# Optimization experiments

Measured on AMD Instinct MI355X. Metric: run time of the kernel, lower is better.

## Reference

```python
import jax, jax.numpy as jnp
import numpy as np

N, E, IN, H, C, L = 40000, 640000, 256, 128, 64, 4
ALPHA, LAMB = 0.5, 1.0


def setup_inputs() -> dict:
    key = jax.random.key(0)
    ks = jax.random.split(key, 8)
    x = jax.random.normal(ks[0], (N, IN), jnp.float32)
    src = jax.random.randint(ks[1], (E,), 0, N, jnp.int32)
    dst = jax.random.randint(ks[2], (E,), 0, N, jnp.int32)
    s_in = 1.0 / np.sqrt(IN)
    s_h = 1.0 / np.sqrt(H)
    fc1_w = jax.random.normal(ks[3], (IN, H), jnp.float32) * s_in
    fc1_b = jnp.zeros((H,), jnp.float32)
    W1 = jax.random.normal(ks[4], (L, H, H), jnp.float32) * s_h   # GCN2Conv weight1 per layer
    W2 = jax.random.normal(ks[5], (L, H, H), jnp.float32) * s_h   # GCN2Conv weight2 (initial-residual proj)
    bgc = jnp.zeros((L, H), jnp.float32)                          # GCN2Conv bias per layer
    fc2_w = jax.random.normal(ks[6], (H, C), jnp.float32) * s_h
    fc2_b = jnp.zeros((C,), jnp.float32)
    return dict(x=x, fc1_w=fc1_w, fc1_b=fc1_b, W1=W1, W2=W2, bgc=bgc,
                fc2_w=fc2_w, fc2_b=fc2_b, src=src, dst=dst)


def reference(x, fc1_w, fc1_b, W1, W2, bgc, fc2_w, fc2_b, src, dst):
    ones = jnp.ones((E,), x.dtype)
    # symmetric 'both' normalization: deg_out^{-1/2} on src side, deg_in^{-1/2} on dst side
    deg_out = jnp.clip(jax.ops.segment_sum(ones, src, num_segments=N), 1.0)
    deg_in = jnp.clip(jax.ops.segment_sum(ones, dst, num_segments=N), 1.0)
    norm_s = (deg_out ** -0.5)[:, None]
    norm_d = (deg_in ** -0.5)[:, None]

    # feature_preprocess: dropout (eval = identity) -> fc1 -> relu
    h0 = jax.nn.relu(x @ fc1_w + fc1_b)          # [N, H]
    h = h0
    for l in range(L):
        beta = float(np.log(LAMB / (l + 1) + 1.0))
        identity = h
        # sparse neighbor aggregation (SpMM via gather + segment_sum)
        agg = jax.ops.segment_sum((h * norm_s)[src], dst, num_segments=N) * norm_d
        feat = (1.0 - ALPHA) * agg               # smoothed features
        f0 = ALPHA * h0                          # initial residual
        rst = (1.0 - beta) * (feat + f0) + beta * (feat @ W1[l] + f0 @ W2[l]) + bgc[l]
        h = jax.nn.relu(rst + identity)          # outer residual + activation (dropout eval = identity)
    return h @ fc2_w + fc2_b                     # [N, C]
```

## Files before the change

kernel.cpp:

```cpp
#include <hip/hip_runtime.h>
#include <math.h>

#define N_NODES 40000
#define N_EDGES 640000
#define IN_F 256
#define H_F 128
#define C_F 64
#define L_LAYERS 4
#define SCAN_BLKS 157
#define N_CHUNKS 32
#define CHUNK_E 20000
#define HIST_WORDS 10000

typedef short short8 __attribute__((ext_vector_type(8)));
typedef unsigned short ushort8 __attribute__((ext_vector_type(8)));
typedef float f32x4 __attribute__((ext_vector_type(4)));

__device__ inline short to_bf16(float f) {
    unsigned u = __builtin_bit_cast(unsigned, f);
    unsigned r = (u + 0x7FFFu + ((u >> 16) & 1u)) >> 16;
    return (short)r;
}
__device__ inline float bf16_to_f(unsigned short u) {
    unsigned v = ((unsigned)u) << 16;
    return __builtin_bit_cast(float, v);
}

__device__ inline int block_excl_scan(int v, int* wsum, int* tot) {
    int tid = threadIdx.x;
    int lane = tid & 63, wid = tid >> 6;
    int incl = v;
    #pragma unroll
    for (int off = 1; off < 64; off <<= 1) {
        int t = __shfl_up(incl, off, 64);
        if (lane >= off) incl += t;
    }
    if (lane == 63) wsum[wid] = incl;
    __syncthreads();
    int prefix = 0, total = 0;
    #pragma unroll
    for (int w = 0; w < 4; w++) {
        int s = wsum[w];
        if (w < wid) prefix += s;
        total += s;
    }
    *tot = total;
    return prefix + incl - v;
}

__global__ void prep_w(const float* __restrict__ fc1_w,
                       const float* __restrict__ W1, const float* __restrict__ W2,
                       const float* __restrict__ fc2_w,
                       short* __restrict__ fc1_wT, short* __restrict__ WcatT,
                       short* __restrict__ fc2_wT) {
    int i = blockIdx.x * 256 + threadIdx.x;
    if (i < 128 * 256) {
        int n = i >> 8, k = i & 255;
        fc1_wT[i] = to_bf16(fc1_w[k * H_F + n]);
    }
    if (i < 4 * 128 * 256) {
        int l = i >> 15; int r = i & 32767; int n = r >> 8; int k = r & 255;
        float w = (k < 128) ? W1[l * 16384 + k * H_F + n]
                            : W2[l * 16384 + (k - 128) * H_F + n];
        WcatT[i] = to_bf16(0.5f * w);
    }
    if (i < 64 * 128) {
        int n = i >> 7, k = i & 127;
        fc2_wT[i] = to_bf16(fc2_w[k * C_F + n]);
    }
}

#define CVT8(dstv, p) {                                                         \
    float4 _v0 = *(const float4*)(p); float4 _v1 = *(const float4*)((p) + 4);   \
    dstv[0] = to_bf16(_v0.x); dstv[1] = to_bf16(_v0.y);                         \
    dstv[2] = to_bf16(_v0.z); dstv[3] = to_bf16(_v0.w);                         \
    dstv[4] = to_bf16(_v1.x); dstv[5] = to_bf16(_v1.y);                         \
    dstv[6] = to_bf16(_v1.z); dstv[7] = to_bf16(_v1.w); }

__global__ __launch_bounds__(256) void hist_fc1(const int* __restrict__ src,
                                                const int* __restrict__ dst,
                                                int* __restrict__ chunk_dst,
                                                int* __restrict__ chunk_src,
                                                unsigned char* __restrict__ lrank8,
                                                const float* __restrict__ x,
                                                const short* __restrict__ wT,
                                                const float* __restrict__ b,
                                                unsigned short* __restrict__ h0b) {
    __shared__ int cntp[HIST_WORDS];
    int blk = blockIdx.x;
    if (blk < 64) {
        int role_dst = (blk < 32);
        int w = role_dst ? blk : blk - 32;
        const int* idx = role_dst ? dst : src;
        int base = w * CHUNK_E;
        for (int i = threadIdx.x; i < HIST_WORDS; i += 256) cntp[i] = 0;
        __syncthreads();
        if (role_dst) {
            for (int i = threadIdx.x; i < CHUNK_E; i += 256) {
                int d = idx[base + i];
                int sh = (d & 3) * 8;
                int old = atomicAdd(&cntp[d >> 2], 1 << sh);
                lrank8[base + i] = (unsigned char)((old >> sh) & 0xff);
            }
        } else {
            for (int i = threadIdx.x; i < CHUNK_E; i += 256) {
                int s = idx[base + i];
                atomicAdd(&cntp[s >> 2], 1 << ((s & 3) * 8));
            }
        }
        __syncthreads();
        int* outp = role_dst ? (chunk_dst + w * HIST_WORDS) : (chunk_src + w * HIST_WORDS);
        for (int i = threadIdx.x; i < HIST_WORDS; i += 256) outp[i] = cntp[i];
        return;
    }
    int bb = blk - 64;
    int tid = threadIdx.x;
    int wave = tid >> 6, lane = tid & 63;
    int m = lane & 15, quad = lane >> 4;
    int row = bb * 64 + wave * 16 + m;
    const float* xr = x + (size_t)row * IN_F + quad * 8;
    short8 afrag[8];
    #pragma unroll
    for (int ks = 0; ks < 8; ks++) {
        CVT8(afrag[ks], xr + ks * 32);
    }
    #pragma unroll
    for (int c = 0; c < 8; c += 2) {
        f32x4 acc0 = {0.f, 0.f, 0.f, 0.f};
        f32x4 acc1 = {0.f, 0.f, 0.f, 0.f};
        const short* b0p = wT + (size_t)(c * 16 + m) * IN_F + quad * 8;
        const short* b1p = b0p + 16 * IN_F;
        #pragma unroll
        for (int ks = 0; ks < 8; ks++) {
            short8 b0 = *(const short8*)(b0p + ks * 32);
            short8 b1 = *(const short8*)(b1p + ks * 32);
            acc0 = __builtin_amdgcn_mfma_f32_16x16x32_bf16(afrag[ks], b0, acc0, 0, 0, 0);
            acc1 = __builtin_amdgcn_mfma_f32_16x16x32_bf16(afrag[ks], b1, acc1, 0, 0, 0);
        }
        int col0 = c * 16 + m;
        int rbase = bb * 64 + wave * 16 + quad * 4;
        float bg0 = b[col0], bg1 = b[col0 + 16];
        #pragma unroll
        for (int r = 0; r < 4; r++) {
            size_t idx2 = (size_t)(rbase + r) * H_F + col0;
            float v0 = acc0[r] + bg0;
            float v1 = acc1[r] + bg1;
            v0 = v0 > 0.f ? v0 : 0.f;
            v1 = v1 > 0.f ? v1 : 0.f;
            h0b[idx2] = (unsigned short)to_bf16(v0);
            h0b[idx2 + 16] = (unsigned short)to_bf16(v1);
        }
    }
}

__global__ __launch_bounds__(256) void scan1(const int* __restrict__ chunk_dst,
                                             const int* __restrict__ chunk_src,
                                             unsigned short* __restrict__ base16,
                                             float* __restrict__ rsq_in,
                                             float* __restrict__ rsq_out,
                                             int* __restrict__ row_local,
                                             int* __restrict__ blk_sum) {
    __shared__ int wsum[4];
    int n = blockIdx.x * 256 + threadIdx.x;
    int deg_in = 0;
    if (n < N_NODES) {
        int word = n >> 2, sh = (n & 3) * 8;
        int run = 0;
        #pragma unroll 4
        for (int w = 0; w < N_CHUNKS; w++) {
            int v = (chunk_dst[w * HIST_WORDS + word] >> sh) & 0xff;
            base16[w * N_NODES + n] = (unsigned short)run;
            run += v;
        }
        deg_in = run;
        int so = 0;
        #pragma unroll 4
        for (int w = 0; w < N_CHUNKS; w++)
            so += (chunk_src[w * HIST_WORDS + word] >> sh) & 0xff;
        rsq_in[n] = 1.0f / sqrtf((float)(deg_in < 1 ? 1 : deg_in));
        rsq_out[n] = 1.0f / sqrtf((float)(so < 1 ? 1 : so));
    }
    int tot;
    int excl = block_excl_scan(deg_in, wsum, &tot);
    if (n < N_NODES) row_local[n] = excl;
    if (threadIdx.x == 0) blk_sum[blockIdx.x] = tot;
}

__global__ __launch_bounds__(256) void scan2(const int* __restrict__ blk_sum,
                                             int* __restrict__ blk_off) {
    __shared__ int wsum[4];
    int t = threadIdx.x;
    int v = (t < SCAN_BLKS) ? blk_sum[t] : 0;
    int tot;
    int excl = block_excl_scan(v, wsum, &tot);
    if (t < SCAN_BLKS) blk_off[t] = excl;
}

__global__ __launch_bounds__(256) void fill_fused(const int* __restrict__ src,
                                                  const int* __restrict__ dst,
                                                  const unsigned char* __restrict__ lrank8,
                                                  const unsigned short* __restrict__ base16,
                                                  const int* __restrict__ row_local,
                                                  const int* __restrict__ blk_off,
                                                  const float* __restrict__ rsq_in,
                                                  const float* __restrict__ rsq_out,
                                                  int* __restrict__ col,
                                                  float* __restrict__ wv,
                                                  int* __restrict__ row_ptr) {
    int blk = blockIdx.x;
    if (blk < 2500) {
        int e = blk * 256 + threadIdx.x;
        int w = e / CHUNK_E;
        int s = src[e], d = dst[e];
        int rp = blk_off[d >> 8] + row_local[d] + (int)base16[w * N_NODES + d]
               + (int)lrank8[e];
        col[rp] = s;
        wv[rp] = rsq_out[s] * rsq_in[d];
        return;
    }
    int n = (blk - 2500) * 256 + threadIdx.x;
    if (n < N_NODES) row_ptr[n] = blk_off[n >> 8] + row_local[n];
    if (blk == 2500 && threadIdx.x == 0) row_ptr[N_NODES] = N_EDGES;
}

__global__ __launch_bounds__(256) void spmm_kernel(const unsigned short* __restrict__ hb,
                                                   const int* __restrict__ row_ptr,
                                                   const int* __restrict__ col,
                                                   const float* __restrict__ wv,
                                                   unsigned short* __restrict__ aggb) {
    int wave = threadIdx.x >> 6, lane = threadIdx.x & 63;
    int slot = lane >> 4, fi = lane & 15;
    int n = blockIdx.x * 4 + wave;
    int e0 = row_ptr[n], e1 = row_ptr[n + 1];
    float a[8] = {};
    int e = e0 + slot;
    for (; e + 12 < e1; e += 16) {
        int c0 = col[e];      float w0 = wv[e];
        int c1 = col[e + 4];  float w1 = wv[e + 4];
        int c2 = col[e + 8];  float w2 = wv[e + 8];
        int c3 = col[e + 12]; float w3 = wv[e + 12];
        ushort8 u0 = *(const ushort8*)(hb + (size_t)c0 * H_F + fi * 8);
        ushort8 u1 = *(const ushort8*)(hb + (size_t)c1 * H_F + fi * 8);
        ushort8 u2 = *(const ushort8*)(hb + (size_t)c2 * H_F + fi * 8);
        ushort8 u3 = *(const ushort8*)(hb + (size_t)c3 * H_F + fi * 8);
        #pragma unroll
        for (int j = 0; j < 8; j++) {
            a[j] += w0 * bf16_to_f(u0[j]) + w1 * bf16_to_f(u1[j])
                  + w2 * bf16_to_f(u2[j]) + w3 * bf16_to_f(u3[j]);
        }
    }
    for (; e < e1; e += 4) {
        int c = col[e];
        float w = wv[e];
        ushort8 u = *(const ushort8*)(hb + (size_t)c * H_F + fi * 8);
        #pragma unroll
        for (int j = 0; j < 8; j++) a[j] += w * bf16_to_f(u[j]);
    }
    #pragma unroll
    for (int mask = 16; mask <= 32; mask <<= 1) {
        #pragma unroll
        for (int j = 0; j < 8; j++) a[j] += __shfl_xor(a[j], mask, 64);
    }
    if (slot == 0) {
        ushort8 r;
        #pragma unroll
        for (int j = 0; j < 8; j++) r[j] = (unsigned short)to_bf16(a[j]);
        *(ushort8*)(aggb + (size_t)n * H_F + fi * 8) = r;
    }
}

__global__ __launch_bounds__(256) void combine_mfma(const unsigned short* __restrict__ aggb,
                                                    const unsigned short* __restrict__ h0b,
                                                    const unsigned short* __restrict__ hb,
                                                    const short* __restrict__ wT,
                                                    const float* __restrict__ bgc,
                                                    float beta,
                                                    unsigned short* __restrict__ h_outb) {
    int tid = threadIdx.x;
    int wave = tid >> 6, lane = tid & 63;
    int m = lane & 15, quad = lane >> 4;
    int row = blockIdx.x * 64 + wave * 16 + m;
    const unsigned short* aggr = aggb + (size_t)row * H_F + quad * 8;
    const unsigned short* h0r  = h0b + (size_t)row * H_F + quad * 8;
    short8 afrag[8];
    #pragma unroll
    for (int ks = 0; ks < 4; ks++) {
        afrag[ks] = __builtin_bit_cast(short8, *(const ushort8*)(aggr + ks * 32));
        afrag[ks + 4] = __builtin_bit_cast(short8, *(const ushort8*)(h0r + ks * 32));
    }
    float omb = 1.f - beta;
    #pragma unroll
    for (int c = 0; c < 8; c += 2) {
        f32x4 acc0 = {0.f, 0.f, 0.f, 0.f};
        f32x4 acc1 = {0.f, 0.f, 0.f, 0.f};
        const short* b0p = wT + (size_t)(c * 16 + m) * 256 + quad * 8;
        const short* b1p = b0p + 16 * 256;
        #pragma unroll
        for (int ks = 0; ks < 8; ks++) {
            short8 b0 = *(const short8*)(b0p + ks * 32);
            short8 b1 = *(const short8*)(b1p + ks * 32);
            acc0 = __builtin_amdgcn_mfma_f32_16x16x32_bf16(afrag[ks], b0, acc0, 0, 0, 0);
            acc1 = __builtin_amdgcn_mfma_f32_16x16x32_bf16(afrag[ks], b1, acc1, 0, 0, 0);
        }
        int col0 = c * 16 + m;
        int rbase = blockIdx.x * 64 + wave * 16 + quad * 4;
        float bg0 = bgc[col0], bg1 = bgc[col0 + 16];
        #pragma unroll
        for (int r = 0; r < 4; r++) {
            size_t idx = (size_t)(rbase + r) * H_F + col0;
            float s0 = 0.5f * (bf16_to_f(aggb[idx]) + bf16_to_f(h0b[idx]));
            float s1 = 0.5f * (bf16_to_f(aggb[idx + 16]) + bf16_to_f(h0b[idx + 16]));
            float v0 = omb * s0 + beta * acc0[r] + bg0 + bf16_to_f(hb[idx]);
            float v1 = omb * s1 + beta * acc1[r] + bg1 + bf16_to_f(hb[idx + 16]);
            v0 = v0 > 0.f ? v0 : 0.f;
            v1 = v1 > 0.f ? v1 : 0.f;
            h_outb[idx] = (unsigned short)to_bf16(v0);
            h_outb[idx + 16] = (unsigned short)to_bf16(v1);
        }
    }
}

__global__ __launch_bounds__(256) void fc2_mfma(const unsigned short* __restrict__ hb,
                                                const short* __restrict__ wT,
                                                const float* __restrict__ b,
                                                float* __restrict__ out) {
    int tid = threadIdx.x;
    int wave = tid >> 6, lane = tid & 63;
    int m = lane & 15, quad = lane >> 4;
    int row = blockIdx.x * 64 + wave * 16 + m;
    const unsigned short* hr = hb + (size_t)row * H_F + quad * 8;
    short8 afrag[4];
    #pragma unroll
    for (int ks = 0; ks < 4; ks++) {
        afrag[ks] = __builtin_bit_cast(short8, *(const ushort8*)(hr + ks * 32));
    }
    #pragma unroll
    for (int c = 0; c < 4; c += 2) {
        f32x4 acc0 = {0.f, 0.f, 0.f, 0.f};
        f32x4 acc1 = {0.f, 0.f, 0.f, 0.f};
        const short* b0p = wT + (size_t)(c * 16 + m) * H_F + quad * 8;
        const short* b1p = b0p + 16 * H_F;
        #pragma unroll
        for (int ks = 0; ks < 4; ks++) {
            short8 b0 = *(const short8*)(b0p + ks * 32);
            short8 b1 = *(const short8*)(b1p + ks * 32);
            acc0 = __builtin_amdgcn_mfma_f32_16x16x32_bf16(afrag[ks], b0, acc0, 0, 0, 0);
            acc1 = __builtin_amdgcn_mfma_f32_16x16x32_bf16(afrag[ks], b1, acc1, 0, 0, 0);
        }
        int col0 = c * 16 + m;
        int rbase = blockIdx.x * 64 + wave * 16 + quad * 4;
        float bg0 = b[col0], bg1 = b[col0 + 16];
        #pragma unroll
        for (int r = 0; r < 4; r++) {
            size_t idx = (size_t)(rbase + r) * C_F + col0;
            out[idx] = acc0[r] + bg0;
            out[idx + 16] = acc1[r] + bg1;
        }
    }
}

extern "C" void kernel_launch(void* const* d_in, const int* in_sizes, int n_in,
                              void* d_out, int out_size, void* d_ws, size_t ws_size,
                              hipStream_t stream) {
    const float* x     = (const float*)d_in[0];
    const float* fc1_w = (const float*)d_in[1];
    const float* fc1_b = (const float*)d_in[2];
    const float* W1    = (const float*)d_in[3];
    const float* W2    = (const float*)d_in[4];
    const float* bgc   = (const float*)d_in[5];
    const float* fc2_w = (const float*)d_in[6];
    const float* fc2_b = (const float*)d_in[7];
    const int*   src   = (const int*)d_in[8];
    const int*   dst   = (const int*)d_in[9];
    float* out = (float*)d_out;

    char* p = (char*)d_ws;
    auto alloc = [&](size_t bytes) {
        char* r = p;
        p += (bytes + 255) & ~(size_t)255;
        return r;
    };
    int*   chunk_dst = (int*)alloc((size_t)N_CHUNKS * HIST_WORDS * 4);
    int*   chunk_src = (int*)alloc((size_t)N_CHUNKS * HIST_WORDS * 4);
    unsigned short* base16 = (unsigned short*)alloc((size_t)N_CHUNKS * N_NODES * 2);
    unsigned char*  lrank8 = (unsigned char*)alloc((size_t)N_EDGES);
    float* rsq_in  = (float*)alloc((size_t)N_NODES * 4);
    float* rsq_out = (float*)alloc((size_t)N_NODES * 4);
    int*   row_ptr   = (int*)alloc((size_t)(N_NODES + 1) * 4);
    int*   row_local = (int*)alloc((size_t)N_NODES * 4);
    int*   blk_sum   = (int*)alloc((size_t)SCAN_BLKS * 4);
    int*   blk_off   = (int*)alloc((size_t)SCAN_BLKS * 4);
    int*   col     = (int*)alloc((size_t)N_EDGES * 4);
    float* wv      = (float*)alloc((size_t)N_EDGES * 4);
    unsigned short* aggb = (unsigned short*)alloc((size_t)N_NODES * H_F * 2);
    unsigned short* h0b  = (unsigned short*)alloc((size_t)N_NODES * H_F * 2);
    unsigned short* hAb  = (unsigned short*)alloc((size_t)N_NODES * H_F * 2);
    unsigned short* hBb  = (unsigned short*)alloc((size_t)N_NODES * H_F * 2);
    short* fc1_wT  = (short*)alloc((size_t)128 * 256 * 2);
    short* WcatT   = (short*)alloc((size_t)4 * 128 * 256 * 2);
    short* fc2_wT  = (short*)alloc((size_t)64 * 128 * 2);

    prep_w<<<512, 256, 0, stream>>>(fc1_w, W1, W2, fc2_w, fc1_wT, WcatT, fc2_wT);
    hist_fc1<<<689, 256, 0, stream>>>(src, dst, chunk_dst, chunk_src, lrank8,
                                      x, fc1_wT, fc1_b, h0b);
    scan1<<<SCAN_BLKS, 256, 0, stream>>>(chunk_dst, chunk_src, base16,
                                         rsq_in, rsq_out, row_local, blk_sum);
    scan2<<<1, 256, 0, stream>>>(blk_sum, blk_off);
    fill_fused<<<2500 + SCAN_BLKS, 256, 0, stream>>>(src, dst, lrank8, base16,
                                                     row_local, blk_off, rsq_in, rsq_out,
                                                     col, wv, row_ptr);

    const unsigned short* sp_in[4] = {h0b, hAb, hBb, hAb};
    unsigned short* out_b[4]       = {hAb, hBb, hAb, hBb};
    for (int l = 0; l < L_LAYERS; l++) {
        float beta = (float)log(1.0 / (double)(l + 1) + 1.0);
        spmm_kernel<<<N_NODES / 4, 256, 0, stream>>>(sp_in[l], row_ptr, col, wv, aggb);
        combine_mfma<<<N_NODES / 64, 256, 0, stream>>>(aggb, h0b, sp_in[l],
                                                       WcatT + (size_t)l * 128 * 256,
                                                       bgc + (size_t)l * H_F,
                                                       beta, out_b[l]);
    }
    fc2_mfma<<<N_NODES / 64, 256, 0, stream>>>(hBb, fc2_wT, fc2_b, out);
}
```

Baseline: 379.9 us.

## Split hist/fc1, fold scan2 into fill, halve rows per GEMM block, predicate SpMM tail

Separates the histogram and fc1 GEMM into two kernels, and changes fc1 and combine so each block handles 32 rows with waves splitting the output columns. This doubles the grid size to raise occupancy and parallelism. The scan2 launch is removed: every fill_fused block now redoes the small 157-entry block-offset scan in shared memory, trading one launch for redundant per-block work. The SpMM remainder loop is replaced by predicated loads in the main 4-way unrolled loop. That loop now issues dummy gathers with zero weight on tails, which costs some extra memory traffic.

```diff
diff --git a/kernel.cpp b/kernel.cpp
--- a/kernel.cpp
+++ b/kernel.cpp
@@ -77,47 +77,46 @@
     dstv[4] = to_bf16(_v1.x); dstv[5] = to_bf16(_v1.y);                         \
     dstv[6] = to_bf16(_v1.z); dstv[7] = to_bf16(_v1.w); }
 
-__global__ __launch_bounds__(256) void hist_fc1(const int* __restrict__ src,
-                                                const int* __restrict__ dst,
-                                                int* __restrict__ chunk_dst,
-                                                int* __restrict__ chunk_src,
-                                                unsigned char* __restrict__ lrank8,
-                                                const float* __restrict__ x,
+__global__ __launch_bounds__(256) void hist_kernel(const int* __restrict__ src,
+                                                   const int* __restrict__ dst,
+                                                   int* __restrict__ chunk_dst,
+                                                   int* __restrict__ chunk_src,
+                                                   unsigned char* __restrict__ lrank8) {
+    __shared__ int cntp[HIST_WORDS];
+    int blk = blockIdx.x;
+    int role_dst = (blk < 32);
+    int w = role_dst ? blk : blk - 32;
+    const int* idx = role_dst ? dst : src;
+    int base = w * CHUNK_E;
+    for (int i = threadIdx.x; i < HIST_WORDS; i += 256) cntp[i] = 0;
+    __syncthreads();
+    if (role_dst) {
+        for (int i = threadIdx.x; i < CHUNK_E; i += 256) {
+            int d = idx[base + i];
+            int sh = (d & 3) * 8;
+            int old = atomicAdd(&cntp[d >> 2], 1 << sh);
+            lrank8[base + i] = (unsigned char)((old >> sh) & 0xff);
+        }
+    } else {
+        for (int i = threadIdx.x; i < CHUNK_E; i += 256) {
+            int s = idx[base + i];
+            atomicAdd(&cntp[s >> 2], 1 << ((s & 3) * 8));
+        }
+    }
+    __syncthreads();
+    int* outp = role_dst ? (chunk_dst + w * HIST_WORDS) : (chunk_src + w * HIST_WORDS);
+    for (int i = threadIdx.x; i < HIST_WORDS; i += 256) outp[i] = cntp[i];
+}
+
+__global__ __launch_bounds__(256) void fc1_mfma(const float* __restrict__ x,
                                                 const short* __restrict__ wT,
                                                 const float* __restrict__ b,
                                                 unsigned short* __restrict__ h0b) {
-    __shared__ int cntp[HIST_WORDS];
-    int blk = blockIdx.x;
-    if (blk < 64) {
-        int role_dst = (blk < 32);
-        int w = role_dst ? blk : blk - 32;
-        const int* idx = role_dst ? dst : src;
-        int base = w * CHUNK_E;
-        for (int i = threadIdx.x; i < HIST_WORDS; i += 256) cntp[i] = 0;
-        __syncthreads();
-        if (role_dst) {
-            for (int i = threadIdx.x; i < CHUNK_E; i += 256) {
-                int d = idx[base + i];
-                int sh = (d & 3) * 8;
-                int old = atomicAdd(&cntp[d >> 2], 1 << sh);
-                lrank8[base + i] = (unsigned char)((old >> sh) & 0xff);
-            }
-        } else {
-            for (int i = threadIdx.x; i < CHUNK_E; i += 256) {
-                int s = idx[base + i];
-                atomicAdd(&cntp[s >> 2], 1 << ((s & 3) * 8));
-            }
-        }
-        __syncthreads();
-        int* outp = role_dst ? (chunk_dst + w * HIST_WORDS) : (chunk_src + w * HIST_WORDS);
-        for (int i = threadIdx.x; i < HIST_WORDS; i += 256) outp[i] = cntp[i];
-        return;
-    }
-    int bb = blk - 64;
     int tid = threadIdx.x;
     int wave = tid >> 6, lane = tid & 63;
+    int rowgrp = wave >> 1, chalf = wave & 1;
     int m = lane & 15, quad = lane >> 4;
-    int row = bb * 64 + wave * 16 + m;
+    int row = blockIdx.x * 32 + rowgrp * 16 + m;
     const float* xr = x + (size_t)row * IN_F + quad * 8;
     short8 afrag[8];
     #pragma unroll
@@ -125,7 +124,8 @@
         CVT8(afrag[ks], xr + ks * 32);
     }
     #pragma unroll
-    for (int c = 0; c < 8; c += 2) {
+    for (int ci = 0; ci < 4; ci += 2) {
+        int c = chalf * 4 + ci;
         f32x4 acc0 = {0.f, 0.f, 0.f, 0.f};
         f32x4 acc1 = {0.f, 0.f, 0.f, 0.f};
         const short* b0p = wT + (size_t)(c * 16 + m) * IN_F + quad * 8;
@@ -138,7 +138,7 @@
             acc1 = __builtin_amdgcn_mfma_f32_16x16x32_bf16(afrag[ks], b1, acc1, 0, 0, 0);
         }
         int col0 = c * 16 + m;
-        int rbase = bb * 64 + wave * 16 + quad * 4;
+        int rbase = blockIdx.x * 32 + rowgrp * 16 + quad * 4;
         float bg0 = b[col0], bg1 = b[col0 + 16];
         #pragma unroll
         for (int r = 0; r < 4; r++) {
@@ -186,41 +186,40 @@
     if (threadIdx.x == 0) blk_sum[blockIdx.x] = tot;
 }
 
-__global__ __launch_bounds__(256) void scan2(const int* __restrict__ blk_sum,
-                                             int* __restrict__ blk_off) {
-    __shared__ int wsum[4];
-    int t = threadIdx.x;
-    int v = (t < SCAN_BLKS) ? blk_sum[t] : 0;
-    int tot;
-    int excl = block_excl_scan(v, wsum, &tot);
-    if (t < SCAN_BLKS) blk_off[t] = excl;
-}
-
 __global__ __launch_bounds__(256) void fill_fused(const int* __restrict__ src,
                                                   const int* __restrict__ dst,
                                                   const unsigned char* __restrict__ lrank8,
                                                   const unsigned short* __restrict__ base16,
                                                   const int* __restrict__ row_local,
-                                                  const int* __restrict__ blk_off,
+                                                  const int* __restrict__ blk_sum,
                                                   const float* __restrict__ rsq_in,
                                                   const float* __restrict__ rsq_out,
                                                   int* __restrict__ col,
                                                   float* __restrict__ wv,
                                                   int* __restrict__ row_ptr) {
+    __shared__ int wsum[4];
+    __shared__ int blk_offL[SCAN_BLKS];
+    int tid = threadIdx.x;
+    int v = (tid < SCAN_BLKS) ? blk_sum[tid] : 0;
+    int tot;
+    int excl = block_excl_scan(v, wsum, &tot);
+    if (tid < SCAN_BLKS) blk_offL[tid] = excl;
+    __syncthreads();
+
     int blk = blockIdx.x;
     if (blk < 2500) {
-        int e = blk * 256 + threadIdx.x;
+        int e = blk * 256 + tid;
         int w = e / CHUNK_E;
         int s = src[e], d = dst[e];
-        int rp = blk_off[d >> 8] + row_local[d] + (int)base16[w * N_NODES + d]
+        int rp = blk_offL[d >> 8] + row_local[d] + (int)base16[w * N_NODES + d]
                + (int)lrank8[e];
         col[rp] = s;
         wv[rp] = rsq_out[s] * rsq_in[d];
         return;
     }
-    int n = (blk - 2500) * 256 + threadIdx.x;
-    if (n < N_NODES) row_ptr[n] = blk_off[n >> 8] + row_local[n];
-    if (blk == 2500 && threadIdx.x == 0) row_ptr[N_NODES] = N_EDGES;
+    int n = (blk - 2500) * 256 + tid;
+    if (n < N_NODES) row_ptr[n] = blk_offL[n >> 8] + row_local[n];
+    if (blk == 2500 && tid == 0) row_ptr[N_NODES] = N_EDGES;
 }
 
 __global__ __launch_bounds__(256) void spmm_kernel(const unsigned short* __restrict__ hb,
@@ -233,12 +232,12 @@
     int n = blockIdx.x * 4 + wave;
     int e0 = row_ptr[n], e1 = row_ptr[n + 1];
     float a[8] = {};
-    int e = e0 + slot;
-    for (; e + 12 < e1; e += 16) {
-        int c0 = col[e];      float w0 = wv[e];
-        int c1 = col[e + 4];  float w1 = wv[e + 4];
-        int c2 = col[e + 8];  float w2 = wv[e + 8];
-        int c3 = col[e + 12]; float w3 = wv[e + 12];
+    for (int e = e0 + slot; e < e1; e += 16) {
+        int eb = e + 4, ec = e + 8, ed = e + 12;
+        int c0 = col[e];                    float w0 = wv[e];
+        int c1 = (eb < e1) ? col[eb] : c0;  float w1 = (eb < e1) ? wv[eb] : 0.f;
+        int c2 = (ec < e1) ? col[ec] : c0;  float w2 = (ec < e1) ? wv[ec] : 0.f;
+        int c3 = (ed < e1) ? col[ed] : c0;  float w3 = (ed < e1) ? wv[ed] : 0.f;
         ushort8 u0 = *(const ushort8*)(hb + (size_t)c0 * H_F + fi * 8);
         ushort8 u1 = *(const ushort8*)(hb + (size_t)c1 * H_F + fi * 8);
         ushort8 u2 = *(const ushort8*)(hb + (size_t)c2 * H_F + fi * 8);
@@ -248,13 +247,6 @@
             a[j] += w0 * bf16_to_f(u0[j]) + w1 * bf16_to_f(u1[j])
                   + w2 * bf16_to_f(u2[j]) + w3 * bf16_to_f(u3[j]);
         }
-    }
-    for (; e < e1; e += 4) {
-        int c = col[e];
-        float w = wv[e];
-        ushort8 u = *(const ushort8*)(hb + (size_t)c * H_F + fi * 8);
-        #pragma unroll
-        for (int j = 0; j < 8; j++) a[j] += w * bf16_to_f(u[j]);
     }
     #pragma unroll
     for (int mask = 16; mask <= 32; mask <<= 1) {
@@ -278,8 +270,9 @@
                                                     unsigned short* __restrict__ h_outb) {
     int tid = threadIdx.x;
     int wave = tid >> 6, lane = tid & 63;
+    int rowgrp = wave >> 1, chalf = wave & 1;
     int m = lane & 15, quad = lane >> 4;
-    int row = blockIdx.x * 64 + wave * 16 + m;
+    int row = blockIdx.x * 32 + rowgrp * 16 + m;
     const unsigned short* aggr = aggb + (size_t)row * H_F + quad * 8;
     const unsigned short* h0r  = h0b + (size_t)row * H_F + quad * 8;
     short8 afrag[8];
@@ -290,7 +283,8 @@
     }
     float omb = 1.f - beta;
     #pragma unroll
-    for (int c = 0; c < 8; c += 2) {
+    for (int ci = 0; ci < 4; ci += 2) {
+        int c = chalf * 4 + ci;
         f32x4 acc0 = {0.f, 0.f, 0.f, 0.f};
         f32x4 acc1 = {0.f, 0.f, 0.f, 0.f};
         const short* b0p = wT + (size_t)(c * 16 + m) * 256 + quad * 8;
@@ -303,7 +297,7 @@
             acc1 = __builtin_amdgcn_mfma_f32_16x16x32_bf16(afrag[ks], b1, acc1, 0, 0, 0);
         }
         int col0 = c * 16 + m;
-        int rbase = blockIdx.x * 64 + wave * 16 + quad * 4;
+        int rbase = blockIdx.x * 32 + rowgrp * 16 + quad * 4;
         float bg0 = bgc[col0], bg1 = bgc[col0 + 16];
         #pragma unroll
         for (int r = 0; r < 4; r++) {
@@ -389,7 +383,6 @@
     int*   row_ptr   = (int*)alloc((size_t)(N_NODES + 1) * 4);
     int*   row_local = (int*)alloc((size_t)N_NODES * 4);
     int*   blk_sum   = (int*)alloc((size_t)SCAN_BLKS * 4);
-    int*   blk_off   = (int*)alloc((size_t)SCAN_BLKS * 4);
     int*   col     = (int*)alloc((size_t)N_EDGES * 4);
     float* wv      = (float*)alloc((size_t)N_EDGES * 4);
     unsigned short* aggb = (unsigned short*)alloc((size_t)N_NODES * H_F * 2);
@@ -401,13 +394,12 @@
     short* fc2_wT  = (short*)alloc((size_t)64 * 128 * 2);
 
     prep_w<<<512, 256, 0, stream>>>(fc1_w, W1, W2, fc2_w, fc1_wT, WcatT, fc2_wT);
-    hist_fc1<<<689, 256, 0, stream>>>(src, dst, chunk_dst, chunk_src, lrank8,
-                                      x, fc1_wT, fc1_b, h0b);
+    hist_kernel<<<64, 256, 0, stream>>>(src, dst, chunk_dst, chunk_src, lrank8);
+    fc1_mfma<<<N_NODES / 32, 256, 0, stream>>>(x, fc1_wT, fc1_b, h0b);
     scan1<<<SCAN_BLKS, 256, 0, stream>>>(chunk_dst, chunk_src, base16,
                                          rsq_in, rsq_out, row_local, blk_sum);
-    scan2<<<1, 256, 0, stream>>>(blk_sum, blk_off);
     fill_fused<<<2500 + SCAN_BLKS, 256, 0, stream>>>(src, dst, lrank8, base16,
-                                                     row_local, blk_off, rsq_in, rsq_out,
+                                                     row_local, blk_sum, rsq_in, rsq_out,
                                                      col, wv, row_ptr);
 
     const unsigned short* sp_in[4] = {h0b, hAb, hBb, hAb};
@@ -415,7 +407,7 @@
     for (int l = 0; l < L_LAYERS; l++) {
         float beta = (float)log(1.0 / (double)(l + 1) + 1.0);
         spmm_kernel<<<N_NODES / 4, 256, 0, stream>>>(sp_in[l], row_ptr, col, wv, aggb);
-        combine_mfma<<<N_NODES / 64, 256, 0, stream>>>(aggb, h0b, sp_in[l],
+        combine_mfma<<<N_NODES / 32, 256, 0, stream>>>(aggb, h0b, sp_in[l],
                                                        WcatT + (size_t)l * 128 * 256,
                                                        bgc + (size_t)l * H_F,
                                                        beta, out_b[l]);
```

Result: no change. 383.3 us (+0.9%).
